# Kernel optimization log

Measured on AMD Instinct MI355X. Metric: run time of the kernel, lower is better.

The kernel has to match this reference:

```python
import jax, jax.numpy as jnp
import numpy as np

B, S, HS = 2, 2048, 2048
H, HKV, D = 16, 4, 128
EPS = 1e-6
NEG = -1e9


def _rms_norm(t, w):
    t32 = t.astype(jnp.float32)
    n = t32 * jax.lax.rsqrt(jnp.mean(t32 * t32, axis=-1, keepdims=True) + EPS)
    return (w.astype(t.dtype) * n.astype(t.dtype))


def _rotate_half(x):
    x1, x2 = jnp.split(x, 2, axis=-1)
    return jnp.concatenate((-x2, x1), axis=-1)


def setup_inputs() -> dict:
    key = jax.random.key(0)
    ks = jax.random.split(key, 6)
    x = jax.random.normal(ks[0], (B, S, HS), dtype=jnp.float32)
    # RoPE tables
    inv_freq = 1.0 / (10000.0 ** (jnp.arange(0, D, 2, dtype=jnp.float32) / D))
    freqs = jnp.arange(S, dtype=jnp.float32)[:, None] * inv_freq[None, :]  # [S, D/2]
    emb = jnp.concatenate((freqs, freqs), axis=-1)  # [S, D]
    cos, sin = jnp.cos(emb), jnp.sin(emb)
    # causal additive mask [1,1,S,S]
    mask = jnp.triu(jnp.full((S, S), NEG, dtype=jnp.float32), k=1)[None, None]
    std = 0.02
    wq = jax.random.normal(ks[1], (H * D, HS), dtype=jnp.float32) * std
    wk = jax.random.normal(ks[2], (HKV * D, HS), dtype=jnp.float32) * std
    wv = jax.random.normal(ks[3], (HKV * D, HS), dtype=jnp.float32) * std
    wo = jax.random.normal(ks[4], (HS, H * D), dtype=jnp.float32) * std
    q_norm_w = jnp.ones((D,), dtype=jnp.float32)
    k_norm_w = jnp.ones((D,), dtype=jnp.float32)
    return {"x": x, "cos": cos, "sin": sin, "mask": mask,
            "wq": wq, "wk": wk, "wv": wv, "wo": wo,
            "q_norm_w": q_norm_w, "k_norm_w": k_norm_w}


def reference(x, cos, sin, mask, wq, wk, wv, wo, q_norm_w, k_norm_w):
    b, s, _ = x.shape
    n_rep = H // HKV
    scale = D ** -0.5
    # QKV projections (torch Linear: y = x @ W^T)
    q = jnp.einsum('bsh,oh->bso', x, wq).reshape(b, s, H, D).transpose(0, 2, 1, 3)
    k = jnp.einsum('bsh,oh->bso', x, wk).reshape(b, s, HKV, D).transpose(0, 2, 1, 3)
    v = jnp.einsum('bsh,oh->bso', x, wv).reshape(b, s, HKV, D).transpose(0, 2, 1, 3)
    # per-head RMS QK-norm
    q = _rms_norm(q, q_norm_w)
    k = _rms_norm(k, k_norm_w)
    # RoPE
    c = cos[None, None]
    sn = sin[None, None]
    q = q * c + _rotate_half(q) * sn
    k = k * c + _rotate_half(k) * sn
    # GQA attention without materializing repeated K/V
    qg = q.reshape(b, HKV, n_rep, s, D)
    scores = jnp.einsum('bhgqd,bhkd->bhgqk', qg, k) * scale + mask  # [b,HKV,G,S,S]
    probs = jax.nn.softmax(scores, axis=-1)
    out = jnp.einsum('bhgqk,bhkd->bhgqd', probs, v)  # [b,HKV,G,S,D]
    out = out.reshape(b, H, s, D).transpose(0, 2, 1, 3).reshape(b, s, H * D)
    return jnp.einsum('bso,ho->bsh', out, wo)
```

## Files before the change

### kernel.cpp

```cpp
#include <hip/hip_runtime.h>
#include <hip/hip_bf16.h>
#include <stdint.h>

typedef unsigned short u16;
typedef __attribute__((ext_vector_type(8))) short short8;
typedef __attribute__((ext_vector_type(4))) float f32x4;
typedef __attribute__((ext_vector_type(4))) unsigned short u16x4;

constexpr int BB = 2, SS = 2048, HSZ = 2048, NH = 16, NKV = 4, DH = 128;
constexpr int MROWS = BB * SS;
constexpr int NQKV = (NH + 2 * NKV) * DH;
constexpr float RMS_EPS = 1e-6f;

__device__ __forceinline__ u16 f2bf(float f) {
  __hip_bfloat16 h = __float2bfloat16(f);
  return *reinterpret_cast<u16*>(&h);
}
__device__ __forceinline__ float bf2f(u16 u) {
  __hip_bfloat16 h;
  *reinterpret_cast<u16*>(&h) = u;
  return __bfloat162float(h);
}

__device__ __forceinline__ void gld16(const void* g, void* l) {
  __builtin_amdgcn_global_load_lds(
      (const __attribute__((address_space(1))) void*)g,
      (__attribute__((address_space(3))) void*)l, 16, 0, 0);
}

constexpr int N_X = MROWS * HSZ;
constexpr int N_WQ = NH * DH * HSZ;
constexpr int N_WK = NKV * DH * HSZ;
constexpr int N_WO = HSZ * HSZ;
__global__ void cvt_all_kernel(const float* __restrict__ x, const float* __restrict__ wq,
                               const float* __restrict__ wk, const float* __restrict__ wv,
                               const float* __restrict__ wo, u16* __restrict__ xb,
                               u16* __restrict__ wqkvb, u16* __restrict__ wob) {
  const int X4 = N_X / 4, Q4 = N_WQ / 4, K4 = N_WK / 4;
  int i = blockIdx.x * blockDim.x + threadIdx.x;
  const float* src;
  u16* dst;
  int off;
  if (i < X4) { src = x; dst = xb; off = i; }
  else if (i < X4 + Q4) { src = wq; dst = wqkvb; off = i - X4; }
  else if (i < X4 + Q4 + K4) { src = wk; dst = wqkvb + N_WQ; off = i - X4 - Q4; }
  else if (i < X4 + Q4 + 2 * K4) { src = wv; dst = wqkvb + N_WQ + N_WK; off = i - X4 - Q4 - K4; }
  else { src = wo; dst = wob; off = i - X4 - Q4 - 2 * K4; }
  float4 v = reinterpret_cast<const float4*>(src)[off];
  u16x4 o;
  o.x = f2bf(v.x); o.y = f2bf(v.y); o.z = f2bf(v.z); o.w = f2bf(v.w);
  reinterpret_cast<u16x4*>(dst)[off] = o;
}

template <typename OutT>
__global__ __launch_bounds__(512, 2) void gemm256(
    const u16* __restrict__ A, const u16* __restrict__ Bm, OutT* __restrict__ C,
    int M, int N, int K, int nbn) {
  __shared__ __align__(16) u16 AS[4][256 * 32];
  __shared__ __align__(16) u16 BS[4][256 * 32];
  const int tid = threadIdx.x;
  const int wave = tid >> 6, lane = tid & 63;
  const int nwg = gridDim.x, bid = blockIdx.x;
  const int wg = (bid & 7) * (nwg >> 3) + (bid >> 3);
  const int bm = wg / nbn, bn = wg % nbn;
  const int row0 = bm * 256, col0 = bn * 256;
  const int wm = wave >> 2, wn = wave & 3;
  const int lr = lane & 15, g = lane >> 4;

  const int rsrc = ((tid >> 5) << 3) | ((tid & 7) ^ ((tid >> 3) & 3));
  const int sce = ((tid >> 3) & 3) << 3;
  const int rxor = g * 128 + (((lr & 7) ^ g) << 4);
  const int abase = (wm * 128) << 6;
  const int bbase = (wn * 64) << 6;

  f32x4 acc[8][4] = {};
  const int niter = K / 64;

#define STG_A(kt, sl, j)                                                      \
  gld16(A + (size_t)(row0 + (j) * 128 + rsrc) * K + (kt) * 32 + sce,          \
        (char*)&AS[sl][0] + (j) * 8192 + wave * 1024)
#define STG_B(kt, sl, j)                                                      \
  gld16(Bm + (size_t)(col0 + (j) * 128 + rsrc) * K + (kt) * 32 + sce,         \
        (char*)&BS[sl][0] + (j) * 8192 + wave * 1024)

  STG_A(0, 0, 0); STG_A(0, 0, 1); STG_B(0, 0, 0); STG_B(0, 0, 1);
  STG_A(1, 1, 0); STG_A(1, 1, 1); STG_B(1, 1, 0); STG_B(1, 1, 1);
  asm volatile("s_waitcnt vmcnt(4)" ::: "memory");
  __builtin_amdgcn_s_barrier();

  for (int it = 0; it < niter; it++) {
    const bool stg = (it + 1) < niter;
    const int slA = (2 * it) & 3, slB = (2 * it + 1) & 3;
    const int ktS = 2 * it + 2;
    const int ss0 = ktS & 3, ss1 = (ktS + 1) & 3;
    const char* Ab = (const char*)&AS[slA][0];
    const char* Bb = (const char*)&BS[slA][0];
    short8 bf[4], af[4];

#pragma unroll
    for (int n = 0; n < 4; n++)
      bf[n] = *(const short8*)(Bb + bbase + ((n * 16 + (lr & 8)) << 6) + rxor);
#pragma unroll
    for (int m = 0; m < 4; m++)
      af[m] = *(const short8*)(Ab + abase + ((m * 16 + (lr & 8)) << 6) + rxor);
    if (stg) { STG_A(ktS, ss0, 0); STG_A(ktS, ss0, 1); }
    __builtin_amdgcn_s_barrier();
    asm volatile("s_waitcnt lgkmcnt(0)" ::: "memory");
    __builtin_amdgcn_sched_barrier(0);
    __builtin_amdgcn_s_setprio(1);
#pragma unroll
    for (int m = 0; m < 4; m++)
#pragma unroll
      for (int n = 0; n < 4; n++)
        acc[m][n] = __builtin_amdgcn_mfma_f32_16x16x32_bf16(af[m], bf[n], acc[m][n], 0, 0, 0);
    __builtin_amdgcn_s_setprio(0);
    __builtin_amdgcn_s_barrier();

#pragma unroll
    for (int m = 0; m < 4; m++)
      af[m] = *(const short8*)(Ab + abase + ((64 + m * 16 + (lr & 8)) << 6) + rxor);
    if (stg) { STG_B(ktS, ss0, 0); STG_B(ktS, ss0, 1); }
    __builtin_amdgcn_s_barrier();
    asm volatile("s_waitcnt lgkmcnt(0)" ::: "memory");
    __builtin_amdgcn_sched_barrier(0);
    __builtin_amdgcn_s_setprio(1);
#pragma unroll
    for (int m = 0; m < 4; m++)
#pragma unroll
      for (int n = 0; n < 4; n++)
        acc[4 + m][n] = __builtin_amdgcn_mfma_f32_16x16x32_bf16(af[m], bf[n], acc[4 + m][n], 0, 0, 0);
    __builtin_amdgcn_s_setprio(0);
    if (stg) asm volatile("s_waitcnt vmcnt(4)" ::: "memory");
    else     asm volatile("s_waitcnt vmcnt(0)" ::: "memory");
    __builtin_amdgcn_s_barrier();

    Ab = (const char*)&AS[slB][0];
    Bb = (const char*)&BS[slB][0];
#pragma unroll
    for (int n = 0; n < 4; n++)
      bf[n] = *(const short8*)(Bb + bbase + ((n * 16 + (lr & 8)) << 6) + rxor);
#pragma unroll
    for (int m = 0; m < 4; m++)
      af[m] = *(const short8*)(Ab + abase + ((m * 16 + (lr & 8)) << 6) + rxor);
    if (stg) { STG_A(ktS + 1, ss1, 0); STG_A(ktS + 1, ss1, 1); }
    __builtin_amdgcn_s_barrier();
    asm volatile("s_waitcnt lgkmcnt(0)" ::: "memory");
    __builtin_amdgcn_sched_barrier(0);
    __builtin_amdgcn_s_setprio(1);
#pragma unroll
    for (int m = 0; m < 4; m++)
#pragma unroll
      for (int n = 0; n < 4; n++)
        acc[m][n] = __builtin_amdgcn_mfma_f32_16x16x32_bf16(af[m], bf[n], acc[m][n], 0, 0, 0);
    __builtin_amdgcn_s_setprio(0);
    __builtin_amdgcn_s_barrier();

#pragma unroll
    for (int m = 0; m < 4; m++)
      af[m] = *(const short8*)(Ab + abase + ((64 + m * 16 + (lr & 8)) << 6) + rxor);
    if (stg) { STG_B(ktS + 1, ss1, 0); STG_B(ktS + 1, ss1, 1); }
    __builtin_amdgcn_s_barrier();
    asm volatile("s_waitcnt lgkmcnt(0)" ::: "memory");
    __builtin_amdgcn_sched_barrier(0);
    __builtin_amdgcn_s_setprio(1);
#pragma unroll
    for (int m = 0; m < 4; m++)
#pragma unroll
      for (int n = 0; n < 4; n++)
        acc[4 + m][n] = __builtin_amdgcn_mfma_f32_16x16x32_bf16(af[m], bf[n], acc[4 + m][n], 0, 0, 0);
    __builtin_amdgcn_s_setprio(0);
    if (stg) asm volatile("s_waitcnt vmcnt(4)" ::: "memory");
    __builtin_amdgcn_s_barrier();
  }
#undef STG_A
#undef STG_B

  const int cr = g * 4, cc = lr;
#pragma unroll
  for (int m = 0; m < 8; m++) {
#pragma unroll
    for (int n = 0; n < 4; n++) {
#pragma unroll
      for (int r = 0; r < 4; r++) {
        size_t idx = (size_t)(row0 + wm * 128 + m * 16 + cr + r) * N +
                     (col0 + wn * 64 + n * 16 + cc);
        if constexpr (sizeof(OutT) == 2) C[idx] = (OutT)f2bf(acc[m][n][r]);
        else C[idx] = acc[m][n][r];
      }
    }
  }
}

__global__ __launch_bounds__(256) void postproc_kernel(
    const u16* __restrict__ Cqkv, const float* __restrict__ cosT,
    const float* __restrict__ sinT, const float* __restrict__ qw,
    const float* __restrict__ kw, u16* __restrict__ qO, u16* __restrict__ kO,
    u16* __restrict__ vO) {
  const int row = blockIdx.x;
  const int b = row / SS, s = row % SS;
  const int wave = threadIdx.x >> 6, lane = threadIdx.x & 63;
  const u16* base = Cqkv + (size_t)row * NQKV;
  const int d0 = lane * 2;
  const float ATT_SCALE = 0.08838834764831843f * 1.4426950408889634f;
  for (int hd = wave; hd < NH + 2 * NKV; hd += 4) {
    const u16* hp = base + hd * DH;
    ushort2 raw = *(const ushort2*)(hp + d0);
    if (hd < NH + NKV) {
      float v0 = bf2f(raw.x), v1 = bf2f(raw.y);
      float ss = v0 * v0 + v1 * v1;
#pragma unroll
      for (int off = 32; off > 0; off >>= 1) ss += __shfl_xor(ss, off);
      float inv = rsqrtf(ss * (1.0f / DH) + RMS_EPS);
      const float* w = (hd < NH) ? qw : kw;
      float n0 = v0 * inv * w[d0], n1 = v1 * inv * w[d0 + 1];
      float r0 = __shfl_xor(n0, 32), r1 = __shfl_xor(n1, 32);
      float sgn = (lane < 32) ? -1.f : 1.f;
      float c0 = cosT[s * DH + d0], c1 = cosT[s * DH + d0 + 1];
      float s0 = sinT[s * DH + d0], s1 = sinT[s * DH + d0 + 1];
      float o0 = n0 * c0 + sgn * r0 * s0;
      float o1 = n1 * c1 + sgn * r1 * s1;
      ushort2 o;
      if (hd < NH) {
        o.x = f2bf(o0 * ATT_SCALE);
        o.y = f2bf(o1 * ATT_SCALE);
        *(ushort2*)(qO + ((size_t)((b * NH + hd) * SS + s)) * DH + d0) = o;
      } else {
        o.x = f2bf(o0);
        o.y = f2bf(o1);
        *(ushort2*)(kO + ((size_t)((b * NKV + hd - NH) * SS + s)) * DH + d0) = o;
      }
    } else {
      *(ushort2*)(vO + ((size_t)((b * NKV + hd - NH - NKV) * SS + s)) * DH + d0) = raw;
    }
  }
}

__global__ __launch_bounds__(256) void transpose_v_kernel(const u16* __restrict__ v,
                                                          u16* __restrict__ vt) {
  __shared__ u16 tile[64][68];
  const int bh = blockIdx.z;
  const int st = blockIdx.x * 64;
  const int dt = blockIdx.y * 64;
  const int tid = threadIdx.x;
  const u16* src = v + ((size_t)bh * SS + st) * DH + dt;
#pragma unroll
  for (int it = 0; it < 4; it++) {
    int r = (tid >> 4) + it * 16, c = (tid & 15) * 4;
    *(u16x4*)&tile[r][c] = *(const u16x4*)(src + (size_t)r * DH + c);
  }
  __syncthreads();
  u16* dst = vt + ((size_t)bh * DH + dt) * SS + st;
#pragma unroll
  for (int it = 0; it < 4; it++) {
    int r2 = (tid >> 4) + it * 16, c2 = (tid & 15) * 4;
    u16x4 o;
    o.x = tile[c2][r2]; o.y = tile[c2 + 1][r2];
    o.z = tile[c2 + 2][r2]; o.w = tile[c2 + 3][r2];
    *(u16x4*)(dst + (size_t)r2 * SS + c2) = o;
  }
}

__global__ __launch_bounds__(256, 2) void attn_kernel(
    const u16* __restrict__ Q, const u16* __restrict__ Kb,
    const u16* __restrict__ Vt, u16* __restrict__ O) {
  __shared__ __align__(16) u16 Ks[64 * 128];
  __shared__ __align__(16) u16 Vs[128 * 64];
  __shared__ __align__(16) u16 Plds[4][16 * 64];
  const int pid = blockIdx.x, h = blockIdx.y, b = blockIdx.z;
  const int hkv = h >> 2;
  const int tid = threadIdx.x;
  const int wave = tid >> 6, lane = tid & 63;
  const int lr = lane & 15, g = lane >> 4;
  const u16* qbase = Q + ((size_t)(b * NH + h) * SS) * DH;
  const u16* kbase = Kb + ((size_t)(b * NKV + hkv) * SS) * DH;
  const u16* vbase = Vt + ((size_t)(b * NKV + hkv) * DH) * SS;

  const int krow = tid >> 4;
  const int kcol = (tid & 15) * 8;
  const int kswz = kcol ^ ((krow & 7) << 3);
  const int vrow = tid >> 3;
  const int vcol = (tid & 7) * 8;
  const int vswz = vcol ^ ((vrow & 7) << 3);
  const int kx = (lr & 7) << 3;
  const int psw = (lr & 7) << 4;
  char* pl = (char*)&Plds[wave][0];

  int4 kr0, kr1, kr2, kr3, vr0, vr1, vr2, vr3;
#define STAGE_LOAD(T)                                                         \
  {                                                                           \
    const int kv0_ = (T) * 64;                                                \
    kr0 = *(const int4*)(kbase + (size_t)(kv0_ + krow) * DH + kcol);          \
    kr1 = *(const int4*)(kbase + (size_t)(kv0_ + krow + 16) * DH + kcol);     \
    kr2 = *(const int4*)(kbase + (size_t)(kv0_ + krow + 32) * DH + kcol);     \
    kr3 = *(const int4*)(kbase + (size_t)(kv0_ + krow + 48) * DH + kcol);     \
    vr0 = *(const int4*)(vbase + (size_t)(vrow) * SS + kv0_ + vcol);          \
    vr1 = *(const int4*)(vbase + (size_t)(vrow + 32) * SS + kv0_ + vcol);     \
    vr2 = *(const int4*)(vbase + (size_t)(vrow + 64) * SS + kv0_ + vcol);     \
    vr3 = *(const int4*)(vbase + (size_t)(vrow + 96) * SS + kv0_ + vcol);     \
  }
#define STAGE_WRITE()                                                         \
  {                                                                           \
    *(int4*)&Ks[(krow) * DH + kswz] = kr0;                                    \
    *(int4*)&Ks[(krow + 16) * DH + kswz] = kr1;                               \
    *(int4*)&Ks[(krow + 32) * DH + kswz] = kr2;                               \
    *(int4*)&Ks[(krow + 48) * DH + kswz] = kr3;                               \
    *(int4*)&Vs[(vrow) * 64 + vswz] = vr0;                                    \
    *(int4*)&Vs[(vrow + 32) * 64 + vswz] = vr1;                               \
    *(int4*)&Vs[(vrow + 64) * 64 + vswz] = vr2;                               \
    *(int4*)&Vs[(vrow + 96) * 64 + vswz] = vr3;                               \
  }

#pragma unroll 1
  for (int half = 0; half < 2; half++) {
    const int qt = half ? (SS / 64 - 1 - pid) : pid;
    const int q0 = qt * 64 + wave * 16;
    const int nt = qt + 1;

    short8 qf[4];
#pragma unroll
    for (int c = 0; c < 4; c++)
      qf[c] = *(const short8*)(qbase + (size_t)(q0 + lr) * DH + c * 32 + g * 8);

    f32x4 o_acc[8] = {};
    float l_run = 0.f;

    STAGE_LOAD(0);
    STAGE_WRITE();
    __syncthreads();

    for (int t = 0; t < nt; t++) {
      const int kv0 = t * 64;
      if (t + 1 < nt) STAGE_LOAD(t + 1);

      f32x4 sf[4] = {};
      __builtin_amdgcn_s_setprio(1);
#pragma unroll
      for (int n = 0; n < 4; n++) {
#pragma unroll
        for (int c = 0; c < 4; c++) {
          short8 kf = *(const short8*)&Ks[(n * 16 + lr) * DH + ((c * 32 + g * 8) ^ kx)];
          sf[n] = __builtin_amdgcn_mfma_f32_16x16x32_bf16(kf, qf[c], sf[n], 0, 0, 0);
        }
      }
      __builtin_amdgcn_s_setprio(0);

      const int qabs = q0 + lr;
      float p[4][4];
      float rs = 0.f;
#pragma unroll
      for (int n = 0; n < 4; n++) {
#pragma unroll
        for (int r = 0; r < 4; r++) {
          const int kvabs = kv0 + n * 16 + g * 4 + r;
          float e = exp2f(sf[n][r] - 17.312340490667562f);
          e = (kvabs <= qabs) ? e : 0.f;
          p[n][r] = e;
          rs += e;
        }
      }
      rs += __shfl_xor(rs, 16);
      rs += __shfl_xor(rs, 32);
      l_run += rs;

#pragma unroll
      for (int n = 0; n < 4; n++) {
        uint2 wv;
        wv.x = (unsigned)f2bf(p[n][0]) | ((unsigned)f2bf(p[n][1]) << 16);
        wv.y = (unsigned)f2bf(p[n][2]) | ((unsigned)f2bf(p[n][3]) << 16);
        *(uint2*)(pl + lr * 128 + ((32 * n + 8 * g) ^ psw)) = wv;
      }

      __builtin_amdgcn_s_setprio(1);
#pragma unroll
      for (int c2 = 0; c2 < 2; c2++) {
        short8 pf = *(const short8*)(pl + lr * 128 + ((64 * c2 + 16 * g) ^ psw));
#pragma unroll
        for (int n2 = 0; n2 < 8; n2++) {
          short8 vf = *(const short8*)&Vs[(n2 * 16 + lr) * 64 + ((c2 * 32 + g * 8) ^ kx)];
          o_acc[n2] = __builtin_amdgcn_mfma_f32_16x16x32_bf16(pf, vf, o_acc[n2], 0, 0, 0);
        }
      }
      __builtin_amdgcn_s_setprio(0);

      __syncthreads();
      if (t + 1 < nt) STAGE_WRITE();
      __syncthreads();
    }

#pragma unroll
    for (int r = 0; r < 4; r++) {
      const float ls = __shfl(l_run, (g << 4) | (g * 4 + r));
      const float inv = 1.0f / ls;
      u16* orow = O + ((size_t)(b * SS + q0 + g * 4 + r)) * (NH * DH) + h * DH;
#pragma unroll
      for (int n2 = 0; n2 < 8; n2++) orow[n2 * 16 + lr] = f2bf(o_acc[n2][r] * inv);
    }
  }
#undef STAGE_LOAD
#undef STAGE_WRITE
}

extern "C" void kernel_launch(void* const* d_in, const int* in_sizes, int n_in,
                              void* d_out, int out_size, void* d_ws, size_t ws_size,
                              hipStream_t stream) {
  const float* x    = (const float*)d_in[0];
  const float* cosT = (const float*)d_in[1];
  const float* sinT = (const float*)d_in[2];
  const float* wq = (const float*)d_in[4];
  const float* wk = (const float*)d_in[5];
  const float* wv = (const float*)d_in[6];
  const float* wo = (const float*)d_in[7];
  const float* qw = (const float*)d_in[8];
  const float* kw = (const float*)d_in[9];
  float* out = (float*)d_out;

  char* p = (char*)d_ws;
  u16* xb    = (u16*)p; p += (size_t)MROWS * HSZ * 2;
  u16* wqkvb = (u16*)p; p += (size_t)NQKV * HSZ * 2;
  u16* wob   = (u16*)p; p += (size_t)HSZ * HSZ * 2;
  u16* cqkv  = (u16*)p; p += (size_t)MROWS * NQKV * 2;
  u16* qb    = (u16*)p; p += (size_t)BB * NH * SS * DH * 2;
  u16* kb    = (u16*)p; p += (size_t)BB * NKV * SS * DH * 2;
  u16* vb    = (u16*)p; p += (size_t)BB * NKV * SS * DH * 2;
  u16* vtb   = (u16*)p; p += (size_t)BB * NKV * SS * DH * 2;
  u16* aob   = (u16*)p; p += (size_t)MROWS * HSZ * 2;

  const int ncvt4 = (N_X + N_WQ + 2 * N_WK + N_WO) / 4;
  cvt_all_kernel<<<dim3(ncvt4 / 256), dim3(256), 0, stream>>>(
      x, wq, wk, wv, wo, xb, wqkvb, wob);

  gemm256<u16><<<dim3((MROWS / 256) * (NQKV / 256)), dim3(512), 0, stream>>>(
      xb, wqkvb, cqkv, MROWS, NQKV, HSZ, NQKV / 256);
  postproc_kernel<<<dim3(MROWS), dim3(256), 0, stream>>>(cqkv, cosT, sinT, qw, kw, qb, kb, vb);
  transpose_v_kernel<<<dim3(SS / 64, DH / 64, BB * NKV), dim3(256), 0, stream>>>(vb, vtb);
  attn_kernel<<<dim3(SS / 128, NH, BB), dim3(256), 0, stream>>>(qb, kb, vtb, aob);
  gemm256<float><<<dim3((MROWS / 256) * (HSZ / 256)), dim3(512), 0, stream>>>(
      aob, wob, out, MROWS, HSZ, HSZ, HSZ / 256);
}
```

Before: 366.1 us.

## Template GEMM tile shape, simplify pipeline, use 256x128 tiles for output projection, skip mask off-diagonal

The GEMM kernel is templated on the N tile width and wave layout. Its main loop is rewritten as two identical phases, each with a single barrier, in place of four sub-steps that each carried several barriers. The output projection now uses 256x128 tiles, doubling the workgroup count from 128 to 256 so the GPU is better filled. The attention kernel applies the causal mask only on the diagonal KV tile, removing compare/select work on the other tiles. The risks are lower per-tile data reuse for the smaller tile and different LDS hazard behaviour from the reduced barrier count.

```diff
diff --git a/kernel.cpp b/kernel.cpp
--- a/kernel.cpp
+++ b/kernel.cpp
@@ -26,6 +26,13 @@
   __builtin_amdgcn_global_load_lds(
       (const __attribute__((address_space(1))) void*)g,
       (__attribute__((address_space(3))) void*)l, 16, 0, 0);
+}
+
+template <int N>
+__device__ __forceinline__ void wait_vmcnt() {
+  if constexpr (N == 0) asm volatile("s_waitcnt vmcnt(0)" ::: "memory");
+  else if constexpr (N == 3) asm volatile("s_waitcnt vmcnt(3)" ::: "memory");
+  else if constexpr (N == 4) asm volatile("s_waitcnt vmcnt(4)" ::: "memory");
 }
 
 constexpr int N_X = MROWS * HSZ;
@@ -52,138 +59,93 @@
   reinterpret_cast<u16x4*>(dst)[off] = o;
 }
 
-template <typename OutT>
+template <int BN, int WM, typename OutT>
 __global__ __launch_bounds__(512, 2) void gemm256(
     const u16* __restrict__ A, const u16* __restrict__ Bm, OutT* __restrict__ C,
     int M, int N, int K, int nbn) {
+  constexpr int WN = 8 / WM;
+  constexpr int MF = (256 / WM) / 16;
+  constexpr int NFr = (BN / WN) / 16;
+  constexpr int BL = BN / 128;
+  constexpr int LPT = 2 + BL;
   __shared__ __align__(16) u16 AS[4][256 * 32];
-  __shared__ __align__(16) u16 BS[4][256 * 32];
+  __shared__ __align__(16) u16 BS[4][BN * 32];
   const int tid = threadIdx.x;
   const int wave = tid >> 6, lane = tid & 63;
   const int nwg = gridDim.x, bid = blockIdx.x;
   const int wg = (bid & 7) * (nwg >> 3) + (bid >> 3);
   const int bm = wg / nbn, bn = wg % nbn;
-  const int row0 = bm * 256, col0 = bn * 256;
-  const int wm = wave >> 2, wn = wave & 3;
+  const int row0 = bm * 256, col0 = bn * BN;
+  const int wm = wave / WN, wn = wave % WN;
   const int lr = lane & 15, g = lane >> 4;
 
   const int rsrc = ((tid >> 5) << 3) | ((tid & 7) ^ ((tid >> 3) & 3));
   const int sce = ((tid >> 3) & 3) << 3;
   const int rxor = g * 128 + (((lr & 7) ^ g) << 4);
-  const int abase = (wm * 128) << 6;
-  const int bbase = (wn * 64) << 6;
-
-  f32x4 acc[8][4] = {};
+  const int abase = (wm * (256 / WM)) << 6;
+  const int bbase = (wn * (BN / WN)) << 6;
+
+  const u16* Ar0 = A + (size_t)(row0 + rsrc) * K + sce;
+  const u16* Ar1 = A + (size_t)(row0 + 128 + rsrc) * K + sce;
+  const u16* Br0 = Bm + (size_t)(col0 + rsrc) * K + sce;
+  const u16* Br1 = Bm + (size_t)(col0 + 128 + rsrc) * K + sce;
+
+  auto stage = [&](int kt, int sl) {
+    char* Ab = (char*)&AS[sl][0] + wave * 1024;
+    char* Bb = (char*)&BS[sl][0] + wave * 1024;
+    gld16(Ar0 + kt * 32, Ab);
+    gld16(Ar1 + kt * 32, Ab + 8192);
+    gld16(Br0 + kt * 32, Bb);
+    if constexpr (BL == 2) gld16(Br1 + kt * 32, Bb + 8192);
+  };
+
+  f32x4 acc[MF][NFr] = {};
   const int niter = K / 64;
 
-#define STG_A(kt, sl, j)                                                      \
-  gld16(A + (size_t)(row0 + (j) * 128 + rsrc) * K + (kt) * 32 + sce,          \
-        (char*)&AS[sl][0] + (j) * 8192 + wave * 1024)
-#define STG_B(kt, sl, j)                                                      \
-  gld16(Bm + (size_t)(col0 + (j) * 128 + rsrc) * K + (kt) * 32 + sce,         \
-        (char*)&BS[sl][0] + (j) * 8192 + wave * 1024)
-
-  STG_A(0, 0, 0); STG_A(0, 0, 1); STG_B(0, 0, 0); STG_B(0, 0, 1);
-  STG_A(1, 1, 0); STG_A(1, 1, 1); STG_B(1, 1, 0); STG_B(1, 1, 1);
-  asm volatile("s_waitcnt vmcnt(4)" ::: "memory");
+  stage(0, 0);
+  stage(1, 1);
+  wait_vmcnt<LPT>();
   __builtin_amdgcn_s_barrier();
+  __builtin_amdgcn_sched_barrier(0);
 
   for (int it = 0; it < niter; it++) {
     const bool stg = (it + 1) < niter;
-    const int slA = (2 * it) & 3, slB = (2 * it + 1) & 3;
-    const int ktS = 2 * it + 2;
-    const int ss0 = ktS & 3, ss1 = (ktS + 1) & 3;
-    const char* Ab = (const char*)&AS[slA][0];
-    const char* Bb = (const char*)&BS[slA][0];
-    short8 bf[4], af[4];
-
-#pragma unroll
-    for (int n = 0; n < 4; n++)
-      bf[n] = *(const short8*)(Bb + bbase + ((n * 16 + (lr & 8)) << 6) + rxor);
-#pragma unroll
-    for (int m = 0; m < 4; m++)
-      af[m] = *(const short8*)(Ab + abase + ((m * 16 + (lr & 8)) << 6) + rxor);
-    if (stg) { STG_A(ktS, ss0, 0); STG_A(ktS, ss0, 1); }
-    __builtin_amdgcn_s_barrier();
-    asm volatile("s_waitcnt lgkmcnt(0)" ::: "memory");
-    __builtin_amdgcn_sched_barrier(0);
-    __builtin_amdgcn_s_setprio(1);
-#pragma unroll
-    for (int m = 0; m < 4; m++)
-#pragma unroll
-      for (int n = 0; n < 4; n++)
-        acc[m][n] = __builtin_amdgcn_mfma_f32_16x16x32_bf16(af[m], bf[n], acc[m][n], 0, 0, 0);
-    __builtin_amdgcn_s_setprio(0);
-    __builtin_amdgcn_s_barrier();
-
-#pragma unroll
-    for (int m = 0; m < 4; m++)
-      af[m] = *(const short8*)(Ab + abase + ((64 + m * 16 + (lr & 8)) << 6) + rxor);
-    if (stg) { STG_B(ktS, ss0, 0); STG_B(ktS, ss0, 1); }
-    __builtin_amdgcn_s_barrier();
-    asm volatile("s_waitcnt lgkmcnt(0)" ::: "memory");
-    __builtin_amdgcn_sched_barrier(0);
-    __builtin_amdgcn_s_setprio(1);
-#pragma unroll
-    for (int m = 0; m < 4; m++)
-#pragma unroll
-      for (int n = 0; n < 4; n++)
-        acc[4 + m][n] = __builtin_amdgcn_mfma_f32_16x16x32_bf16(af[m], bf[n], acc[4 + m][n], 0, 0, 0);
-    __builtin_amdgcn_s_setprio(0);
-    if (stg) asm volatile("s_waitcnt vmcnt(4)" ::: "memory");
-    else     asm volatile("s_waitcnt vmcnt(0)" ::: "memory");
-    __builtin_amdgcn_s_barrier();
-
-    Ab = (const char*)&AS[slB][0];
-    Bb = (const char*)&BS[slB][0];
-#pragma unroll
-    for (int n = 0; n < 4; n++)
-      bf[n] = *(const short8*)(Bb + bbase + ((n * 16 + (lr & 8)) << 6) + rxor);
-#pragma unroll
-    for (int m = 0; m < 4; m++)
-      af[m] = *(const short8*)(Ab + abase + ((m * 16 + (lr & 8)) << 6) + rxor);
-    if (stg) { STG_A(ktS + 1, ss1, 0); STG_A(ktS + 1, ss1, 1); }
-    __builtin_amdgcn_s_barrier();
-    asm volatile("s_waitcnt lgkmcnt(0)" ::: "memory");
-    __builtin_amdgcn_sched_barrier(0);
-    __builtin_amdgcn_s_setprio(1);
-#pragma unroll
-    for (int m = 0; m < 4; m++)
-#pragma unroll
-      for (int n = 0; n < 4; n++)
-        acc[m][n] = __builtin_amdgcn_mfma_f32_16x16x32_bf16(af[m], bf[n], acc[m][n], 0, 0, 0);
-    __builtin_amdgcn_s_setprio(0);
-    __builtin_amdgcn_s_barrier();
-
-#pragma unroll
-    for (int m = 0; m < 4; m++)
-      af[m] = *(const short8*)(Ab + abase + ((64 + m * 16 + (lr & 8)) << 6) + rxor);
-    if (stg) { STG_B(ktS + 1, ss1, 0); STG_B(ktS + 1, ss1, 1); }
-    __builtin_amdgcn_s_barrier();
-    asm volatile("s_waitcnt lgkmcnt(0)" ::: "memory");
-    __builtin_amdgcn_sched_barrier(0);
-    __builtin_amdgcn_s_setprio(1);
-#pragma unroll
-    for (int m = 0; m < 4; m++)
-#pragma unroll
-      for (int n = 0; n < 4; n++)
-        acc[4 + m][n] = __builtin_amdgcn_mfma_f32_16x16x32_bf16(af[m], bf[n], acc[4 + m][n], 0, 0, 0);
-    __builtin_amdgcn_s_setprio(0);
-    if (stg) asm volatile("s_waitcnt vmcnt(4)" ::: "memory");
-    __builtin_amdgcn_s_barrier();
-  }
-#undef STG_A
-#undef STG_B
+#pragma unroll
+    for (int ph = 0; ph < 2; ph++) {
+      const int kt = 2 * it + ph;
+      const char* Ab = (const char*)&AS[kt & 3][0];
+      const char* Bb = (const char*)&BS[kt & 3][0];
+      short8 af[MF], bf[NFr];
+#pragma unroll
+      for (int m = 0; m < MF; m++)
+        af[m] = *(const short8*)(Ab + abase + ((m * 16 + (lr & 8)) << 6) + rxor);
+#pragma unroll
+      for (int n = 0; n < NFr; n++)
+        bf[n] = *(const short8*)(Bb + bbase + ((n * 16 + (lr & 8)) << 6) + rxor);
+      if (stg) stage(kt + 2, (kt + 2) & 3);
+      __builtin_amdgcn_s_setprio(1);
+#pragma unroll
+      for (int m = 0; m < MF; m++)
+#pragma unroll
+        for (int n = 0; n < NFr; n++)
+          acc[m][n] = __builtin_amdgcn_mfma_f32_16x16x32_bf16(af[m], bf[n], acc[m][n], 0, 0, 0);
+      __builtin_amdgcn_s_setprio(0);
+      if (stg) wait_vmcnt<LPT>();
+      else if (ph == 0) wait_vmcnt<0>();
+      __builtin_amdgcn_s_barrier();
+      __builtin_amdgcn_sched_barrier(0);
+    }
+  }
 
   const int cr = g * 4, cc = lr;
 #pragma unroll
-  for (int m = 0; m < 8; m++) {
-#pragma unroll
-    for (int n = 0; n < 4; n++) {
+  for (int m = 0; m < MF; m++) {
+#pragma unroll
+    for (int n = 0; n < NFr; n++) {
 #pragma unroll
       for (int r = 0; r < 4; r++) {
-        size_t idx = (size_t)(row0 + wm * 128 + m * 16 + cr + r) * N +
-                     (col0 + wn * 64 + n * 16 + cc);
+        size_t idx = (size_t)(row0 + wm * (256 / WM) + m * 16 + cr + r) * N +
+                     (col0 + wn * (BN / WN) + n * 16 + cc);
         if constexpr (sizeof(OutT) == 2) C[idx] = (OutT)f2bf(acc[m][n][r]);
         else C[idx] = acc[m][n][r];
       }
@@ -329,7 +291,6 @@
     __syncthreads();
 
     for (int t = 0; t < nt; t++) {
-      const int kv0 = t * 64;
       if (t + 1 < nt) STAGE_LOAD(t + 1);
 
       f32x4 sf[4] = {};
@@ -344,19 +305,30 @@
       }
       __builtin_amdgcn_s_setprio(0);
 
-      const int qabs = q0 + lr;
       float p[4][4];
       float rs = 0.f;
-#pragma unroll
-      for (int n = 0; n < 4; n++) {
-#pragma unroll
-        for (int r = 0; r < 4; r++) {
-          const int kvabs = kv0 + n * 16 + g * 4 + r;
-          float e = exp2f(sf[n][r] - 17.312340490667562f);
-          e = (kvabs <= qabs) ? e : 0.f;
-          p[n][r] = e;
-          rs += e;
-        }
+      if (t + 1 < nt) {
+#pragma unroll
+        for (int n = 0; n < 4; n++)
+#pragma unroll
+          for (int r = 0; r < 4; r++) {
+            float e = exp2f(sf[n][r] - 17.312340490667562f);
+            p[n][r] = e;
+            rs += e;
+          }
+      } else {
+        const int qabs = q0 + lr;
+        const int kvb = t * 64;
+#pragma unroll
+        for (int n = 0; n < 4; n++)
+#pragma unroll
+          for (int r = 0; r < 4; r++) {
+            const int kvabs = kvb + n * 16 + g * 4 + r;
+            float e = exp2f(sf[n][r] - 17.312340490667562f);
+            e = (kvabs <= qabs) ? e : 0.f;
+            p[n][r] = e;
+            rs += e;
+          }
       }
       rs += __shfl_xor(rs, 16);
       rs += __shfl_xor(rs, 32);
@@ -429,11 +401,11 @@
   cvt_all_kernel<<<dim3(ncvt4 / 256), dim3(256), 0, stream>>>(
       x, wq, wk, wv, wo, xb, wqkvb, wob);
 
-  gemm256<u16><<<dim3((MROWS / 256) * (NQKV / 256)), dim3(512), 0, stream>>>(
+  gemm256<256, 2, u16><<<dim3((MROWS / 256) * (NQKV / 256)), dim3(512), 0, stream>>>(
       xb, wqkvb, cqkv, MROWS, NQKV, HSZ, NQKV / 256);
   postproc_kernel<<<dim3(MROWS), dim3(256), 0, stream>>>(cqkv, cosT, sinT, qw, kw, qb, kb, vb);
   transpose_v_kernel<<<dim3(SS / 64, DH / 64, BB * NKV), dim3(256), 0, stream>>>(vb, vtb);
   attn_kernel<<<dim3(SS / 128, NH, BB), dim3(256), 0, stream>>>(qb, kb, vtb, aob);
-  gemm256<float><<<dim3((MROWS / 256) * (HSZ / 256)), dim3(512), 0, stream>>>(
-      aob, wob, out, MROWS, HSZ, HSZ, HSZ / 256);
-}
+  gemm256<128, 4, float><<<dim3((MROWS / 256) * (HSZ / 128)), dim3(512), 0, stream>>>(
+      aob, wob, out, MROWS, HSZ, HSZ, HSZ / 128);
+}
```

Result: faster. 338.1 us (-7.7%).
